# Kernel tuning notes

Measured on AMD Instinct MI355X. Metric: run time of the kernel, lower is better.

The kernel has to match this reference:

```python
import jax, jax.numpy as jnp
import numpy as np


def setup_inputs() -> dict:
    key = jax.random.key(0)
    k1, k2 = jax.random.split(key)
    N, M, D = 8192, 8192, 512
    x = jax.random.normal(k1, (N, D), dtype=jnp.float32)
    y = jax.random.normal(k2, (M, D), dtype=jnp.float32)
    gamma = jnp.float32(1.0)
    return {"x": x, "y": y, "gamma": gamma}


def reference(x, y, gamma):
    # k(x, y) = exp(-gamma * ||x - y||^2)
    x = x.reshape(-1, x.shape[-1])
    y = y.reshape(-1, y.shape[-1])
    x_sq = jnp.sum(x * x, axis=-1)  # [N]
    y_sq = jnp.sum(y * y, axis=-1)  # [M]
    cross = x @ y.T                  # [N, M]
    sq_dist = x_sq[:, None] + y_sq[None, :] - 2.0 * cross
    sq_dist = jnp.maximum(sq_dist, 0.0)  # guard tiny negative roundoff
    return jnp.exp(-gamma * sq_dist)
```

## Files before the change

### kernel.cpp

```cpp
#include <hip/hip_runtime.h>
#include <hip/hip_bf16.h>

typedef unsigned short u16;
typedef __attribute__((ext_vector_type(8))) short bf16x8;
typedef __attribute__((ext_vector_type(4))) float f32x4;

typedef const __attribute__((address_space(1))) void gvoid_t;
typedef __attribute__((address_space(3))) void lvoid_t;

__device__ __forceinline__ void gload_lds16(const void* g, void* l) {
  __builtin_amdgcn_global_load_lds((gvoid_t*)g, (lvoid_t*)l, 16, 0, 0);
}

__device__ __forceinline__ u16 f2bf(float f) {
  union { float f; unsigned u; } a;
  a.f = f;
  unsigned r = (a.u + 0x7FFFu + ((a.u >> 16) & 1u)) >> 16;
  return (u16)r;
}

__global__ __launch_bounds__(128) void rbf_prep(
    const float* __restrict__ x, const float* __restrict__ y,
    u16* __restrict__ xb, u16* __restrict__ yb,
    float* __restrict__ xsq, float* __restrict__ ysq,
    int N, int M, int D) {
  int row = blockIdx.x;
  const float* src;
  u16* dst;
  float* sq;
  if (row < N) {
    src = x + (size_t)row * D;
    dst = xb + (size_t)row * D;
    sq = xsq + row;
  } else {
    int r = row - N;
    src = y + (size_t)r * D;
    dst = yb + (size_t)r * D;
    sq = ysq + r;
  }
  int t = threadIdx.x;
  float4 v = reinterpret_cast<const float4*>(src)[t];
  float s = v.x * v.x + v.y * v.y + v.z * v.z + v.w * v.w;
  ushort4 o;
  o.x = f2bf(v.x);
  o.y = f2bf(v.y);
  o.z = f2bf(v.z);
  o.w = f2bf(v.w);
  reinterpret_cast<ushort4*>(dst)[t] = o;
  #pragma unroll
  for (int off = 32; off > 0; off >>= 1) s += __shfl_down(s, off, 64);
  __shared__ float red[2];
  if ((t & 63) == 0) red[t >> 6] = s;
  __syncthreads();
  if (t == 0) sq[0] = red[0] + red[1];
}

#define BM 128
#define BN 128
#define BK 32

__global__ __launch_bounds__(256, 4) void rbf_gemm(
    const u16* __restrict__ xb, const u16* __restrict__ yb,
    const float* __restrict__ xsq, const float* __restrict__ ysq,
    const float* __restrict__ gptr, float* __restrict__ out,
    int N, int M, int D) {
  __shared__ u16 lds[2][2][BM * BK];

  int bid = blockIdx.x;
  int nbr = N / BM, nbc = M / BN;
  int trow, tcol;
  if (nbr == 64 && nbc == 64) {
    int xcd = bid & 7;
    int s = bid >> 3;
    int gr = s >> 6;
    int q = s & 63;
    trow = gr * 8 + (q & 7);
    tcol = xcd * 8 + (q >> 3);
  } else {
    int cpx = gridDim.x >> 3;
    int swz = (bid & 7) * cpx + (bid >> 3);
    trow = swz / nbc;
    tcol = swz % nbc;
  }
  int brow = trow * BM;
  int bcol = tcol * BN;

  int tid = threadIdx.x;
  int w = tid >> 6;
  int lane = tid & 63;
  int wm = w >> 1;
  int wn = w & 1;
  int fr = lane & 15;
  int fq = lane >> 4;

  int srow = lane >> 2;
  int schunk = (lane & 3) * 8;
  const u16* xsrc = xb + (size_t)(brow + w * 32 + srow) * D + schunk;
  const u16* ysrc = yb + (size_t)(bcol + w * 32 + srow) * D + schunk;
  int sdst = w * 1024;

  int colf = fq * 8;
  int arow0 = (wm * 64 + fr) * 32 + colf;
  int brow0 = (wn * 64 + fr) * 32 + colf;

  f32x4 acc[4][4];
  #pragma unroll
  for (int m = 0; m < 4; ++m)
    #pragma unroll
    for (int n = 0; n < 4; ++n)
      acc[m][n] = (f32x4){0.f, 0.f, 0.f, 0.f};

  auto stage = [&](int kt, int b) {
    const u16* xs = xsrc + kt * 32;
    const u16* ys = ysrc + kt * 32;
    u16* la = &lds[b][0][sdst];
    u16* lb = &lds[b][1][sdst];
    gload_lds16(xs, la);
    gload_lds16(xs + (size_t)16 * D, la + 512);
    gload_lds16(ys, lb);
    gload_lds16(ys + (size_t)16 * D, lb + 512);
  };

  int nkt = D >> 5;
  stage(0, 0);
  stage(1, 1);
  for (int t = 0; t < nkt; ++t) {
    int b = t & 1;
    if (t + 1 < nkt)
      asm volatile("s_waitcnt vmcnt(4)" ::: "memory");
    else
      asm volatile("s_waitcnt vmcnt(0)" ::: "memory");
    __builtin_amdgcn_sched_barrier(0);
    __builtin_amdgcn_s_barrier();
    __builtin_amdgcn_sched_barrier(0);

    const u16* A = &lds[b][0][0];
    const u16* B = &lds[b][1][0];
    bf16x8 af[4], bf[4];
    #pragma unroll
    for (int m = 0; m < 4; ++m)
      af[m] = *(const bf16x8*)&A[arow0 + m * 512];
    #pragma unroll
    for (int n = 0; n < 4; ++n)
      bf[n] = *(const bf16x8*)&B[brow0 + n * 512];

    __builtin_amdgcn_s_setprio(1);
    #pragma unroll
    for (int m = 0; m < 4; ++m)
      #pragma unroll
      for (int n = 0; n < 4; ++n)
        acc[m][n] = __builtin_amdgcn_mfma_f32_16x16x32_bf16(
            bf[n], af[m], acc[m][n], 0, 0, 0);
    __builtin_amdgcn_s_setprio(0);

    asm volatile("s_waitcnt lgkmcnt(0)" ::: "memory");
    __builtin_amdgcn_sched_barrier(0);
    __builtin_amdgcn_s_barrier();
    __builtin_amdgcn_sched_barrier(0);
    if (t + 2 < nkt) stage(t + 2, b);
  }

  float gl2 = gptr[0] * 1.44269504088896f;
  float m2gl2 = 2.0f * gl2;
  float4 gys[4];
  #pragma unroll
  for (int n = 0; n < 4; ++n) {
    float4 t4 = *reinterpret_cast<const float4*>(
        &ysq[bcol + wn * 64 + n * 16 + fq * 4]);
    gys[n].x = gl2 * t4.x;
    gys[n].y = gl2 * t4.y;
    gys[n].z = gl2 * t4.z;
    gys[n].w = gl2 * t4.w;
  }
  #pragma unroll
  for (int m = 0; m < 4; ++m) {
    int i = brow + wm * 64 + m * 16 + fr;
    float gxs = gl2 * xsq[i];
    size_t ro = (size_t)i * M;
    #pragma unroll
    for (int n = 0; n < 4; ++n) {
      int jb = bcol + wn * 64 + n * 16 + fq * 4;
      float4 e;
      e.x = exp2f(fminf(fmaf(m2gl2, acc[m][n][0], -(gxs + gys[n].x)), 0.f));
      e.y = exp2f(fminf(fmaf(m2gl2, acc[m][n][1], -(gxs + gys[n].y)), 0.f));
      e.z = exp2f(fminf(fmaf(m2gl2, acc[m][n][2], -(gxs + gys[n].z)), 0.f));
      e.w = exp2f(fminf(fmaf(m2gl2, acc[m][n][3], -(gxs + gys[n].w)), 0.f));
      *reinterpret_cast<float4*>(&out[ro + jb]) = e;
    }
  }
}

__global__ __launch_bounds__(256) void rbf_naive(
    const float* __restrict__ x, const float* __restrict__ y,
    const float* __restrict__ gptr, float* __restrict__ out,
    int N, int M, int D) {
  __shared__ float xs[16][17];
  __shared__ float ys[16][17];
  int nbn = M / 16;
  int brow = (blockIdx.x / nbn) * 16;
  int bcol = (blockIdx.x % nbn) * 16;
  int ti = threadIdx.x >> 4, tj = threadIdx.x & 15;
  float dacc = 0.f, xacc = 0.f, yacc = 0.f;
  for (int k0 = 0; k0 < D; k0 += 16) {
    xs[ti][tj] = x[(size_t)(brow + ti) * D + k0 + tj];
    ys[ti][tj] = y[(size_t)(bcol + ti) * D + k0 + tj];
    __syncthreads();
    #pragma unroll
    for (int kk = 0; kk < 16; ++kk) {
      float xv = xs[ti][kk], yv = ys[tj][kk];
      dacc += xv * yv;
      xacc += xv * xv;
      yacc += yv * yv;
    }
    __syncthreads();
  }
  float gamma = gptr[0];
  float d2 = fmaxf(xacc + yacc - 2.f * dacc, 0.f);
  out[(size_t)(brow + ti) * M + (bcol + tj)] = __expf(-gamma * d2);
}

extern "C" void kernel_launch(void* const* d_in, const int* in_sizes, int n_in,
                              void* d_out, int out_size, void* d_ws,
                              size_t ws_size, hipStream_t stream) {
  const float* x = (const float*)d_in[0];
  const float* y = (const float*)d_in[1];
  const float* g = (const float*)d_in[2];
  float* out = (float*)d_out;

  const int D = 512;
  const int N = in_sizes[0] / D;
  const int M = in_sizes[1] / D;

  size_t need = (size_t)(N + M) * D * sizeof(u16) + (size_t)(N + M) * sizeof(float);
  bool shapes_ok = (N % BM == 0) && (M % BN == 0) && (D % BK == 0) && (D / BK >= 2);

  if (ws_size >= need && shapes_ok) {
    u16* xb = (u16*)d_ws;
    u16* yb = xb + (size_t)N * D;
    float* xsq = (float*)(yb + (size_t)M * D);
    float* ysq = xsq + N;

    rbf_prep<<<N + M, 128, 0, stream>>>(x, y, xb, yb, xsq, ysq, N, M, D);
    int nwg = (N / BM) * (M / BN);
    rbf_gemm<<<nwg, 256, 0, stream>>>(xb, yb, xsq, ysq, g, out, N, M, D);
  } else {
    rbf_naive<<<(N / 16) * (M / 16), 256, 0, stream>>>(x, y, g, out, N, M, D);
  }
}
```

Baseline: 118.4 us.

## Replace LDS-staged GEMM tiles with direct global-to-register fragment loads

Result: slower. 261.0 us (+120.4%).

```diff
diff --git a/kernel.cpp b/kernel.cpp
--- a/kernel.cpp
+++ b/kernel.cpp
@@ -4,13 +4,6 @@
 typedef unsigned short u16;
 typedef __attribute__((ext_vector_type(8))) short bf16x8;
 typedef __attribute__((ext_vector_type(4))) float f32x4;
-
-typedef const __attribute__((address_space(1))) void gvoid_t;
-typedef __attribute__((address_space(3))) void lvoid_t;
-
-__device__ __forceinline__ void gload_lds16(const void* g, void* l) {
-  __builtin_amdgcn_global_load_lds((gvoid_t*)g, (lvoid_t*)l, 16, 0, 0);
-}
 
 __device__ __forceinline__ u16 f2bf(float f) {
   union { float f; unsigned u; } a;
@@ -55,19 +48,13 @@
   if (t == 0) sq[0] = red[0] + red[1];
 }
 
-#define BM 128
-#define BN 128
-#define BK 32
-
-__global__ __launch_bounds__(256, 4) void rbf_gemm(
+__global__ __launch_bounds__(256, 3) void rbf_gemm(
     const u16* __restrict__ xb, const u16* __restrict__ yb,
     const float* __restrict__ xsq, const float* __restrict__ ysq,
     const float* __restrict__ gptr, float* __restrict__ out,
     int N, int M, int D) {
-  __shared__ u16 lds[2][2][BM * BK];
-
   int bid = blockIdx.x;
-  int nbr = N / BM, nbc = M / BN;
+  int nbr = N / 128, nbc = M / 128;
   int trow, tcol;
   if (nbr == 64 && nbc == 64) {
     int xcd = bid & 7;
@@ -82,8 +69,6 @@
     trow = swz / nbc;
     tcol = swz % nbc;
   }
-  int brow = trow * BM;
-  int bcol = tcol * BN;
 
   int tid = threadIdx.x;
   int w = tid >> 6;
@@ -93,15 +78,12 @@
   int fr = lane & 15;
   int fq = lane >> 4;
 
-  int srow = lane >> 2;
-  int schunk = (lane & 3) * 8;
-  const u16* xsrc = xb + (size_t)(brow + w * 32 + srow) * D + schunk;
-  const u16* ysrc = yb + (size_t)(bcol + w * 32 + srow) * D + schunk;
-  int sdst = w * 1024;
-
-  int colf = fq * 8;
-  int arow0 = (wm * 64 + fr) * 32 + colf;
-  int brow0 = (wn * 64 + fr) * 32 + colf;
+  int brow = trow * 128 + wm * 64;
+  int bcol = tcol * 128 + wn * 64;
+
+  const u16* xrow = xb + (size_t)(brow + fr) * D + fq * 8;
+  const u16* yrow = yb + (size_t)(bcol + fr) * D + fq * 8;
+  const size_t rstep = (size_t)16 * D;
 
   f32x4 acc[4][4];
   #pragma unroll
@@ -110,54 +92,42 @@
     for (int n = 0; n < 4; ++n)
       acc[m][n] = (f32x4){0.f, 0.f, 0.f, 0.f};
 
-  auto stage = [&](int kt, int b) {
-    const u16* xs = xsrc + kt * 32;
-    const u16* ys = ysrc + kt * 32;
-    u16* la = &lds[b][0][sdst];
-    u16* lb = &lds[b][1][sdst];
-    gload_lds16(xs, la);
-    gload_lds16(xs + (size_t)16 * D, la + 512);
-    gload_lds16(ys, lb);
-    gload_lds16(ys + (size_t)16 * D, lb + 512);
-  };
-
-  int nkt = D >> 5;
-  stage(0, 0);
-  stage(1, 1);
-  for (int t = 0; t < nkt; ++t) {
-    int b = t & 1;
-    if (t + 1 < nkt)
-      asm volatile("s_waitcnt vmcnt(4)" ::: "memory");
-    else
-      asm volatile("s_waitcnt vmcnt(0)" ::: "memory");
-    __builtin_amdgcn_sched_barrier(0);
-    __builtin_amdgcn_s_barrier();
-    __builtin_amdgcn_sched_barrier(0);
-
-    const u16* A = &lds[b][0][0];
-    const u16* B = &lds[b][1][0];
-    bf16x8 af[4], bf[4];
-    #pragma unroll
-    for (int m = 0; m < 4; ++m)
-      af[m] = *(const bf16x8*)&A[arow0 + m * 512];
-    #pragma unroll
-    for (int n = 0; n < 4; ++n)
-      bf[n] = *(const bf16x8*)&B[brow0 + n * 512];
-
-    __builtin_amdgcn_s_setprio(1);
+  bf16x8 afA[4], bfA[4], afB[4], bfB[4];
+
+  #pragma unroll
+  for (int m = 0; m < 4; ++m) afA[m] = *(const bf16x8*)&xrow[m * rstep];
+  #pragma unroll
+  for (int n = 0; n < 4; ++n) bfA[n] = *(const bf16x8*)&yrow[n * rstep];
+
+  int NK = D >> 5;
+  #pragma unroll 2
+  for (int k = 0; k < NK; k += 2) {
+    int k1 = (k + 1) << 5;
+    #pragma unroll
+    for (int m = 0; m < 4; ++m) afB[m] = *(const bf16x8*)&xrow[m * rstep + k1];
+    #pragma unroll
+    for (int n = 0; n < 4; ++n) bfB[n] = *(const bf16x8*)&yrow[n * rstep + k1];
     #pragma unroll
     for (int m = 0; m < 4; ++m)
       #pragma unroll
       for (int n = 0; n < 4; ++n)
         acc[m][n] = __builtin_amdgcn_mfma_f32_16x16x32_bf16(
-            bf[n], af[m], acc[m][n], 0, 0, 0);
-    __builtin_amdgcn_s_setprio(0);
-
-    asm volatile("s_waitcnt lgkmcnt(0)" ::: "memory");
-    __builtin_amdgcn_sched_barrier(0);
-    __builtin_amdgcn_s_barrier();
-    __builtin_amdgcn_sched_barrier(0);
-    if (t + 2 < nkt) stage(t + 2, b);
+            bfA[n], afA[m], acc[m][n], 0, 0, 0);
+    if (k + 2 < NK) {
+      int k2 = (k + 2) << 5;
+      #pragma unroll
+      for (int m = 0; m < 4; ++m)
+        afA[m] = *(const bf16x8*)&xrow[m * rstep + k2];
+      #pragma unroll
+      for (int n = 0; n < 4; ++n)
+        bfA[n] = *(const bf16x8*)&yrow[n * rstep + k2];
+    }
+    #pragma unroll
+    for (int m = 0; m < 4; ++m)
+      #pragma unroll
+      for (int n = 0; n < 4; ++n)
+        acc[m][n] = __builtin_amdgcn_mfma_f32_16x16x32_bf16(
+            bfB[n], afB[m], acc[m][n], 0, 0, 0);
   }
 
   float gl2 = gptr[0] * 1.44269504088896f;
@@ -165,8 +135,7 @@
   float4 gys[4];
   #pragma unroll
   for (int n = 0; n < 4; ++n) {
-    float4 t4 = *reinterpret_cast<const float4*>(
-        &ysq[bcol + wn * 64 + n * 16 + fq * 4]);
+    float4 t4 = *reinterpret_cast<const float4*>(&ysq[bcol + n * 16 + fq * 4]);
     gys[n].x = gl2 * t4.x;
     gys[n].y = gl2 * t4.y;
     gys[n].z = gl2 * t4.z;
@@ -174,12 +143,12 @@
   }
   #pragma unroll
   for (int m = 0; m < 4; ++m) {
-    int i = brow + wm * 64 + m * 16 + fr;
+    int i = brow + m * 16 + fr;
     float gxs = gl2 * xsq[i];
     size_t ro = (size_t)i * M;
     #pragma unroll
     for (int n = 0; n < 4; ++n) {
-      int jb = bcol + wn * 64 + n * 16 + fq * 4;
+      int jb = bcol + n * 16 + fq * 4;
       float4 e;
       e.x = exp2f(fminf(fmaf(m2gl2, acc[m][n][0], -(gxs + gys[n].x)), 0.f));
       e.y = exp2f(fminf(fmaf(m2gl2, acc[m][n][1], -(gxs + gys[n].y)), 0.f));
@@ -232,7 +201,7 @@
   const int M = in_sizes[1] / D;
 
   size_t need = (size_t)(N + M) * D * sizeof(u16) + (size_t)(N + M) * sizeof(float);
-  bool shapes_ok = (N % BM == 0) && (M % BN == 0) && (D % BK == 0) && (D / BK >= 2);
+  bool shapes_ok = (N % 128 == 0) && (M % 128 == 0) && (D % 64 == 0);
 
   if (ws_size >= need && shapes_ok) {
     u16* xb = (u16*)d_ws;
@@ -241,7 +210,7 @@
     float* ysq = xsq + N;
 
     rbf_prep<<<N + M, 128, 0, stream>>>(x, y, xb, yb, xsq, ysq, N, M, D);
-    int nwg = (N / BM) * (M / BN);
+    int nwg = (N / 128) * (M / 128);
     rbf_gemm<<<nwg, 256, 0, stream>>>(xb, yb, xsq, ysq, g, out, N, M, D);
   } else {
     rbf_naive<<<(N / 16) * (M / 16), 256, 0, stream>>>(x, y, g, out, N, M, D);
```
